# Optimization experiments

Hardware: AMD Instinct MI355X
Metric: run time of the kernel (lower is better)

Reference implementation:

```python
import jax, jax.numpy as jnp
import numpy as np

B, T_IN, T_OUT, N, FEAT = 32, 96, 96, 512, 8
HID = 512
GRID_SIZE, SPLINE_ORDER = 5, 3
GRID_RANGE = (-1.0, 1.0)


def _make_grid():
    # matches KANLinear.create_grid: identical row per in_feature, so keep 1-D
    h = (GRID_RANGE[1] - GRID_RANGE[0]) / GRID_SIZE
    return jnp.arange(-SPLINE_ORDER, GRID_SIZE + SPLINE_ORDER + 1, dtype=jnp.float32) * h + GRID_RANGE[0]


def _b_splines(x, grid):
    # x: [M, in_features]; de Boor-Cox recursion, order SPLINE_ORDER
    x = x[..., None]  # [M, in, 1]
    bases = ((x >= grid[:-1]) & (x < grid[1:])).astype(x.dtype)
    for k in range(1, SPLINE_ORDER + 1):
        left = (x - grid[:-(k + 1)]) / (grid[k:-1] - grid[:-(k + 1)])
        right = (grid[k + 1:] - x) / (grid[k + 1:] - grid[1:-k])
        bases = left * bases[..., :-1] + right * bases[..., 1:]
    return bases  # [M, in, grid_size + spline_order]


def setup_inputs() -> dict:
    key = jax.random.key(0)
    ks = jax.random.split(key, 12)
    s = 0.05
    return {
        "X": jax.random.normal(ks[0], (B, T_IN, N, FEAT), jnp.float32),
        "Y": jax.random.normal(ks[1], (B, T_OUT, N, FEAT), jnp.float32),
        "Wx": jax.random.normal(ks[2], (HID, T_IN * FEAT), jnp.float32) * s,
        "bx": jax.random.normal(ks[3], (HID,), jnp.float32) * s,
        "Wy": jax.random.normal(ks[4], (HID, T_OUT * FEAT), jnp.float32) * s,
        "by": jax.random.normal(ks[5], (HID,), jnp.float32) * s,
        "base_w": jax.random.normal(ks[6], (64, 2 * HID), jnp.float32) * s,
        "spline_w": jax.random.normal(ks[7], (64, 2 * HID, GRID_SIZE + SPLINE_ORDER), jnp.float32) * s,
        "spline_scaler": jax.random.normal(ks[8], (64, 2 * HID), jnp.float32) * s,
        "Wf": jax.random.normal(ks[9], (T_OUT * FEAT, 64), jnp.float32) * s,
        "bf": jax.random.normal(ks[10], (T_OUT * FEAT,), jnp.float32) * s,
    }


def reference(X, Y, Wx, bx, Wy, by, base_w, spline_w, spline_scaler, Wf, bf):
    # [B, T, N, F] -> [B, N, T*F]
    Xf = jnp.transpose(X, (0, 2, 1, 3)).reshape(B, N, T_IN * FEAT)
    Yf = jnp.transpose(Y, (0, 2, 1, 3)).reshape(B, N, T_OUT * FEAT)
    Hx = jnp.tanh(Xf @ Wx.T + bx)
    Hy = jnp.tanh(Yf @ Wy.T + by)
    h = jnp.concatenate([Hx, Hy], axis=-1).reshape(B * N, 2 * HID)

    grid = _make_grid()
    base_out = jax.nn.silu(h) @ base_w.T
    scaled_sw = spline_w * spline_scaler[..., None]  # [out, in, coeff]
    spline_out = jnp.einsum("mik,oik->mo", _b_splines(h, grid), scaled_sw)
    kan_out = (base_out + spline_out).reshape(B, N, 64)

    out = kan_out @ Wf.T + bf  # [B, N, T_OUT*FEAT]
    out = out.reshape(B, N, T_OUT, FEAT)
    return jnp.transpose(out, (0, 2, 1, 3))  # [B, T_OUT, N, FEAT]
```

## Files before the change

kernel.cpp:

```cpp
#include <hip/hip_runtime.h>
#include <cmath>

#define B_    32
#define T_    96
#define N_    512
#define F_    8
#define TF_   768
#define HID_  512
#define M_    16384
#define KIN_  1024
#define KS_   8

typedef short short8 __attribute__((ext_vector_type(8)));
typedef float f32x4  __attribute__((ext_vector_type(4)));
typedef unsigned int  uintx4 __attribute__((ext_vector_type(4)));
typedef unsigned long long ulongx2 __attribute__((ext_vector_type(2)));
typedef _Float16 halfx8 __attribute__((ext_vector_type(8)));
typedef unsigned short      ushort_t;
typedef unsigned int        uint_t;
typedef unsigned long long  ulong_t;

#define HT_B     0ull
#define WQ_B     33554432ull
#define WB_B     34734080ull
#define SH_B     36306944ull
#define KANR_B   61472768ull
#define WFQ_B    63569920ull

static __device__ inline uint_t  fbits(float f){ return __builtin_bit_cast(uint_t, f); }
static __device__ inline ushort_t f2b(float f){
    uint_t u = fbits(f);
    return (ushort_t)((u + 0x7fffu + ((u >> 16) & 1u)) >> 16);
}
static __device__ inline float b2f(ushort_t h){ return __builtin_bit_cast(float, (uint_t)h << 16); }
static __device__ inline ulong_t pack4(float4 v){
    return (ulong_t)f2b(v.x) | ((ulong_t)f2b(v.y) << 16) |
           ((ulong_t)f2b(v.z) << 32) | ((ulong_t)f2b(v.w) << 48);
}
static __device__ inline ulong_t pack4t(float4 v){
    uint_t d0 = (fbits(v.x) >> 16) | (fbits(v.y) & 0xffff0000u);
    uint_t d1 = (fbits(v.z) >> 16) | (fbits(v.w) & 0xffff0000u);
    return (ulong_t)d0 | ((ulong_t)d1 << 32);
}
static __device__ inline float fast_tanh(float x){
    const float e = __expf(2.0f * x);
    return 1.0f - 2.0f / (e + 1.0f);
}
static __device__ inline void gload_lds16(const void* g, void* l){
    __builtin_amdgcn_global_load_lds(
        (const __attribute__((address_space(1))) unsigned int*)g,
        (__attribute__((address_space(3))) unsigned int*)l, 16, 0, 0);
}

__global__ __launch_bounds__(256) void pack_wq(
    const float* __restrict__ base_w,
    const float* __restrict__ spline_w,
    const float* __restrict__ scaler,
    ushort_t* __restrict__ wq)
{
    const int e = blockIdx.x * 256 + threadIdx.x;
    const int j    = e & 7;
    const int ln   = (e >> 3) & 63;
    const int ct   = (e >> 9) & 3;
    const int t    = (e >> 11) & 3;
    const int rest = e >> 13;
    const int ss   = rest % 9;
    const int ks   = rest / 9;
    const int o = ct * 16 + (ln & 15);
    const int g = ln >> 4;
    float v;
    if (ss < 8) {
        const int i = ks * 128 + ss * 16 + t * 4 + g;
        v = spline_w[(o * KIN_ + i) * 8 + j] * scaler[o * KIN_ + i];
    } else {
        const int i = ks * 128 + t * 32 + g * 8 + j;
        v = base_w[o * KIN_ + i];
    }
    wq[e] = f2b(v);
}

__global__ __launch_bounds__(256) void pack_wb2(
    const float* __restrict__ Wx,
    const float* __restrict__ Wy,
    ushort_t* __restrict__ wb)
{
    const int e = blockIdx.x * 256 + threadIdx.x;
    const float v = (e < 512 * TF_) ? Wx[e] : Wy[e - 512 * TF_];
    wb[e] = f2b(v);
}

__global__ __launch_bounds__(256) void pack_wfq(
    const float* __restrict__ Wf, ushort_t* __restrict__ wfq)
{
    const int e = blockIdx.x * 256 + threadIdx.x;
    const int jj  = e & 7;
    const int ln  = (e >> 3) & 63;
    const int rt  = (e >> 9) & 3;
    const int s   = (e >> 11) & 1;
    const int wvt = (e >> 12) & 1;
    const int tb  = e >> 13;
    const int tf = tb * 128 + wvt * 64 + rt * 16 + (ln & 15);
    const int o  = s * 32 + (ln >> 4) * 8 + jj;
    wfq[e] = f2b(Wf[(size_t)tf * 64 + o]);
}

__global__ __launch_bounds__(256) void xcvt_kernel(
    const float* __restrict__ Xs, ushort_t* __restrict__ xbf)
{
    __shared__ __align__(16) char lds[32 * 1552];
    const int tid = threadIdx.x;
    const int n0  = blockIdx.x * 32;
    const int bb  = blockIdx.y;
    const int nl  = (tid & 63) >> 1;
    const int f4  = (tid & 1) * 4;
    const int tq  = tid >> 6;
    #pragma unroll 4
    for (int u = 0; u < 24; u++) {
        const int t = u * 4 + tq;
        const float4 v = *(const float4*)(Xs + (size_t)bb * (T_ * N_ * F_)
                                             + (size_t)t * (N_ * F_)
                                             + (size_t)(n0 + nl) * F_ + f4);
        *(ulong_t*)(lds + nl * 1552 + t * 16 + f4 * 2) = pack4t(v);
    }
    __syncthreads();
    #pragma unroll 4
    for (int u = 0; u < 12; u++) {
        const int c   = u * 256 + tid;
        const int row = c / 96;
        const int col = c - row * 96;
        const uintx4 val = *(const uintx4*)(lds + row * 1552 + col * 16);
        *(uintx4*)(xbf + (size_t)(bb * 512 + n0 + row) * TF_ + col * 8) = val;
    }
}

__global__ __launch_bounds__(512, 2) void gemm_tanh_v7(
    const ushort_t* __restrict__ xbf,
    const ushort_t* __restrict__ wb,
    const float* __restrict__ bias,
    ushort_t* __restrict__ ht, int z)
{
    __shared__ __align__(16) char smem[32768];

    const int tid = threadIdx.x;
    const int wv  = tid >> 6;
    const int ln  = tid & 63;
    const int lr  = ln & 15;
    const int hi  = ln >> 4;
    const int wm  = wv >> 2;
    const int wj  = wv & 3;

    const int m0  = blockIdx.x * 128;
    const int jl0 = blockIdx.y * 128;
    const int j0  = z * 512 + jl0;

    const int r_l = ln >> 3;
    const int ck  = ((ln & 7) ^ r_l) * 8;

    f32x4 acc[4][2] = {};

    for (int kt = 0; kt < 12; kt++) {
        __syncthreads();
        #pragma unroll
        for (int s = 0; s < 2; s++) {
            const int reg = s * 8 + wv;
            const int row = reg * 8 + r_l;
            gload_lds16(xbf + (size_t)(m0 + row) * TF_ + kt * 64 + ck,
                        smem + reg * 1024 + ln * 16);
            gload_lds16(wb + (size_t)(j0 + row) * TF_ + kt * 64 + ck,
                        smem + 16384 + reg * 1024 + ln * 16);
        }
        __syncthreads();

        #pragma unroll
        for (int h = 0; h < 2; h++) {
            const int g = h * 4 + hi;
            short8 a[4], b[2];
            #pragma unroll
            for (int rt = 0; rt < 4; rt++) {
                const int r = wm * 64 + rt * 16 + lr;
                a[rt] = *(short8*)(smem + r * 128 + ((g ^ (r & 7)) * 16));
            }
            #pragma unroll
            for (int ct = 0; ct < 2; ct++) {
                const int r = wj * 32 + ct * 16 + lr;
                b[ct] = *(short8*)(smem + 16384 + r * 128 + ((g ^ (r & 7)) * 16));
            }
            #pragma unroll
            for (int rt = 0; rt < 4; rt++)
                #pragma unroll
                for (int ct = 0; ct < 2; ct++)
                    acc[rt][ct] = __builtin_amdgcn_mfma_f32_16x16x32_bf16(
                        a[rt], b[ct], acc[rt][ct], 0, 0, 0);
        }
    }

    __syncthreads();
    #pragma unroll
    for (int ct = 0; ct < 2; ct++) {
        const int j = wj * 32 + ct * 16 + lr;
        const float bvv = bias[jl0 + j];
        #pragma unroll
        for (int rt = 0; rt < 4; rt++) {
            const f32x4 v = acc[rt][ct];
            float4 tv;
            tv.x = fast_tanh(v[0] + bvv);
            tv.y = fast_tanh(v[1] + bvv);
            tv.z = fast_tanh(v[2] + bvv);
            tv.w = fast_tanh(v[3] + bvv);
            const int slot = wm * 8 + rt * 2 + (hi >> 1);
            *(ulong_t*)(smem + j * 256 + ((slot ^ (j & 15)) * 16) + (hi & 1) * 8)
                = pack4(tv);
        }
    }
    __syncthreads();
    {
        const int j  = tid >> 2;
        const int q4 = tid & 3;
        ushort_t* dst = ht + (size_t)(j0 + j) * M_ + m0 + q4 * 32;
        #pragma unroll
        for (int w = 0; w < 4; w++) {
            const int slot = q4 * 4 + w;
            short8 val = *(short8*)(smem + j * 256 + ((slot ^ (j & 15)) * 16));
            *(short8*)(dst + w * 8) = val;
        }
    }
}

static __device__ inline short8 eval_bases(float x)
{
    const float v = fmaf(x, 2.5f, 2.5f);
    float sf = floorf(v);
    sf = fminf(fmaxf(sf, 0.0f), 4.0f);
    const float u = v - sf;
    const int si = (int)sf;
    const float u2 = u * u, u3 = u2 * u;
    const float omu = 1.0f - u;
    const float omu3 = omu * omu * omu;
    const float Bb0 = omu3 * (1.0f / 6.0f);
    const float Bb3 = u3 * (1.0f / 6.0f);
    const float Bb1 = fmaf(0.5f, u3, 2.0f / 3.0f) - u2;
    const float Bb2 = 1.0f - Bb0 - Bb1 - Bb3;
    const uint_t d0 = (fbits(Bb0) >> 16) | (fbits(Bb1) & 0xffff0000u);
    const uint_t d1 = (fbits(Bb2) >> 16) | (fbits(Bb3) & 0xffff0000u);
    const ulong_t P = (ulong_t)d0 | ((ulong_t)d1 << 32);
    const int sh = si << 4;
    const ulong_t Plo = P << (sh & 63);
    const ulong_t Phi = P >> ((64 - sh) & 63);
    ulongx2 pr;
    pr.x = (si == 4) ? 0ull : Plo;
    pr.y = (si == 0) ? 0ull : ((si == 4) ? P : Phi);
    return __builtin_bit_cast(short8, pr);
}

__global__ __launch_bounds__(256) void kan_v5(
    const ushort_t* __restrict__ ht,
    const ushort_t* __restrict__ wq,
    _Float16* __restrict__ kanp)
{
    const int tid = threadIdx.x;
    const int wv  = tid >> 6;
    const int ln  = tid & 63;
    const int g   = ln >> 4;
    const int lr  = ln & 15;
    const int m0  = blockIdx.x * 64;
    const int ks  = blockIdx.y;
    const int iB  = ks * 128;
    const size_t r0 = (size_t)(m0 + wv * 16 + lr);

    const short8* wqf = (const short8*)wq + (size_t)ks * 9216 + ln;
    const ushort_t* htg  = ht + (size_t)(iB + g) * M_ + r0;
    const ushort_t* htg8 = ht + (size_t)(iB + g * 8) * M_ + r0;

    f32x4 acc[4] = {};

    for (int ss = 0; ss < 8; ss++) {
        #pragma unroll
        for (int t = 0; t < 4; t++) {
            const short8* bp = wqf + (size_t)(ss * 4 + t) * 256;
            const short8 b0 = bp[0], b1 = bp[64], b2 = bp[128], b3 = bp[192];
            const short8 a0 = eval_bases(b2f(htg[(size_t)(ss * 16 + t * 4) * M_]));
            acc[0] = __builtin_amdgcn_mfma_f32_16x16x32_bf16(a0, b0, acc[0], 0, 0, 0);
            acc[1] = __builtin_amdgcn_mfma_f32_16x16x32_bf16(a0, b1, acc[1], 0, 0, 0);
            acc[2] = __builtin_amdgcn_mfma_f32_16x16x32_bf16(a0, b2, acc[2], 0, 0, 0);
            acc[3] = __builtin_amdgcn_mfma_f32_16x16x32_bf16(a0, b3, acc[3], 0, 0, 0);
        }
    }
    #pragma unroll
    for (int t = 0; t < 4; t++) {
        const short8* bp = wqf + (size_t)(32 + t) * 256;
        const short8 b0 = bp[0], b1 = bp[64], b2 = bp[128], b3 = bp[192];
        uintx4 d;
        #pragma unroll
        for (int jj = 0; jj < 4; jj++) {
            const float x0 = b2f(htg8[(size_t)(t * 32 + 2 * jj)     * M_]);
            const float x1 = b2f(htg8[(size_t)(t * 32 + 2 * jj + 1) * M_]);
            const float s0 = x0 / (1.0f + __expf(-x0));
            const float s1 = x1 / (1.0f + __expf(-x1));
            d[jj] = (fbits(s0) >> 16) | (fbits(s1) & 0xffff0000u);
        }
        const short8 a0 = __builtin_bit_cast(short8, d);
        acc[0] = __builtin_amdgcn_mfma_f32_16x16x32_bf16(a0, b0, acc[0], 0, 0, 0);
        acc[1] = __builtin_amdgcn_mfma_f32_16x16x32_bf16(a0, b1, acc[1], 0, 0, 0);
        acc[2] = __builtin_amdgcn_mfma_f32_16x16x32_bf16(a0, b2, acc[2], 0, 0, 0);
        acc[3] = __builtin_amdgcn_mfma_f32_16x16x32_bf16(a0, b3, acc[3], 0, 0, 0);
    }

    #pragma unroll
    for (int ct = 0; ct < 4; ct++) {
        const int o = ct * 16 + lr;
        #pragma unroll
        for (int q = 0; q < 4; q++) {
            const size_t row = (size_t)(m0 + wv * 16 + g * 4 + q);
            kanp[(size_t)ks * (M_ * 64) + row * 64 + o] = (_Float16)acc[ct][q];
        }
    }
}

__global__ __launch_bounds__(256) void reduce_kan(
    const _Float16* __restrict__ kanp, ushort_t* __restrict__ kanr)
{
    const int e8 = blockIdx.x * 256 + threadIdx.x;
    const size_t base = (size_t)e8 * 8;
    float s[8] = {};
    #pragma unroll
    for (int p = 0; p < KS_; p++) {
        const halfx8 v = *(const halfx8*)(kanp + (size_t)p * (M_ * 64) + base);
        #pragma unroll
        for (int j = 0; j < 8; j++) s[j] += (float)v[j];
    }
    float4 s0 = make_float4(s[0], s[1], s[2], s[3]);
    float4 s1 = make_float4(s[4], s[5], s[6], s[7]);
    ulongx2 outv;
    outv.x = pack4(s0);
    outv.y = pack4(s1);
    *(ulongx2*)(kanr + base) = outv;
}

__global__ __launch_bounds__(256) void final_v2(
    const ushort_t* __restrict__ kanr,
    const ushort_t* __restrict__ wfq,
    const float* __restrict__ bf,
    float* __restrict__ out)
{
    const int tid = threadIdx.x;
    const int wv  = tid >> 6;
    const int ln  = tid & 63;
    const int lr  = ln & 15;
    const int hi  = ln >> 4;
    const int wvm = wv >> 1;
    const int wvt = wv & 1;
    const int mb  = blockIdx.x;
    const int tb  = blockIdx.y;

    f32x4 acc[4][4] = {};

    #pragma unroll
    for (int s = 0; s < 2; s++) {
        short8 afr[4], bfr[4];
        #pragma unroll
        for (int rt = 0; rt < 4; rt++) {
            const size_t idx = ((size_t)(((tb * 2 + wvt) * 2 + s) * 4 + rt)) * 64 + ln;
            afr[rt] = ((const short8*)wfq)[idx];
        }
        #pragma unroll
        for (int ct = 0; ct < 4; ct++) {
            const int m = mb * 128 + wvm * 64 + ct * 16 + lr;
            bfr[ct] = *(const short8*)(kanr + (size_t)m * 64 + s * 32 + hi * 8);
        }
        #pragma unroll
        for (int rt = 0; rt < 4; rt++)
            #pragma unroll
            for (int ct = 0; ct < 4; ct++)
                acc[rt][ct] = __builtin_amdgcn_mfma_f32_16x16x32_bf16(
                    afr[rt], bfr[ct], acc[rt][ct], 0, 0, 0);
    }

    #pragma unroll
    for (int rt = 0; rt < 4; rt++) {
        const int tf0 = tb * 128 + wvt * 64 + rt * 16 + hi * 4;
        const float4 b4 = *(const float4*)&bf[tf0];
        const int t  = tf0 >> 3;
        const int f0 = tf0 & 7;
        #pragma unroll
        for (int ct = 0; ct < 4; ct++) {
            const int m = mb * 128 + wvm * 64 + ct * 16 + lr;
            const int bb = m >> 9;
            const int n  = m & 511;
            const f32x4 v = acc[rt][ct];
            float4 o4 = make_float4(v[0] + b4.x, v[1] + b4.y, v[2] + b4.z, v[3] + b4.w);
            *(float4*)&out[(size_t)bb * (T_ * N_ * F_)
                           + (size_t)t * (N_ * F_)
                           + (size_t)n * F_ + f0] = o4;
        }
    }
}

extern "C" void kernel_launch(void* const* d_in, const int* in_sizes, int n_in,
                              void* d_out, int out_size, void* d_ws, size_t ws_size,
                              hipStream_t stream)
{
    const float* X      = (const float*)d_in[0];
    const float* Y      = (const float*)d_in[1];
    const float* Wx     = (const float*)d_in[2];
    const float* bx     = (const float*)d_in[3];
    const float* Wy     = (const float*)d_in[4];
    const float* by     = (const float*)d_in[5];
    const float* base_w = (const float*)d_in[6];
    const float* spline_w = (const float*)d_in[7];
    const float* spline_scaler = (const float*)d_in[8];
    const float* Wf     = (const float*)d_in[9];
    const float* bf     = (const float*)d_in[10];

    float* out = (float*)d_out;
    ushort_t* ht   = (ushort_t*)((char*)d_ws + HT_B);
    ushort_t* wq   = (ushort_t*)((char*)d_ws + WQ_B);
    ushort_t* wb   = (ushort_t*)((char*)d_ws + WB_B);
    ushort_t* xbf  = (ushort_t*)((char*)d_ws + SH_B);
    _Float16* kanp = (_Float16*)((char*)d_ws + SH_B);
    ushort_t* kanr = (ushort_t*)((char*)d_ws + KANR_B);
    ushort_t* wfq  = (ushort_t*)((char*)d_ws + WFQ_B);

    pack_wq<<<2304, 256, 0, stream>>>(base_w, spline_w, spline_scaler, wq);
    pack_wb2<<<3072, 256, 0, stream>>>(Wx, Wy, wb);
    pack_wfq<<<192, 256, 0, stream>>>(Wf, wfq);

    xcvt_kernel<<<dim3(16, 32), 256, 0, stream>>>(X, xbf);
    gemm_tanh_v7<<<dim3(128, 4), 512, 0, stream>>>(xbf, wb, bx, ht, 0);
    xcvt_kernel<<<dim3(16, 32), 256, 0, stream>>>(Y, xbf);
    gemm_tanh_v7<<<dim3(128, 4), 512, 0, stream>>>(xbf, wb, by, ht, 1);

    kan_v5<<<dim3(M_ / 64, KS_), 256, 0, stream>>>(ht, wq, kanp);
    reduce_kan<<<512, 256, 0, stream>>>(kanp, kanr);
    final_v2<<<dim3(128, 6), 256, 0, stream>>>(kanr, wfq, bf, out);
}
```

Before: 144.6 us.

## Stage KAN weights in LDS, double row tile, fold split-K reduction into final GEMM

Result: slower. 151.9 us (+5.0%).

```diff
diff --git a/kernel.cpp b/kernel.cpp
--- a/kernel.cpp
+++ b/kernel.cpp
@@ -12,10 +12,10 @@
 #define KS_   8
 
 typedef short short8 __attribute__((ext_vector_type(8)));
+typedef _Float16 half8 __attribute__((ext_vector_type(8)));
 typedef float f32x4  __attribute__((ext_vector_type(4)));
 typedef unsigned int  uintx4 __attribute__((ext_vector_type(4)));
 typedef unsigned long long ulongx2 __attribute__((ext_vector_type(2)));
-typedef _Float16 halfx8 __attribute__((ext_vector_type(8)));
 typedef unsigned short      ushort_t;
 typedef unsigned int        uint_t;
 typedef unsigned long long  ulong_t;
@@ -24,7 +24,6 @@
 #define WQ_B     33554432ull
 #define WB_B     34734080ull
 #define SH_B     36306944ull
-#define KANR_B   61472768ull
 #define WFQ_B    63569920ull
 
 static __device__ inline uint_t  fbits(float f){ return __builtin_bit_cast(uint_t, f); }
@@ -89,8 +88,8 @@
     wb[e] = f2b(v);
 }
 
-__global__ __launch_bounds__(256) void pack_wfq(
-    const float* __restrict__ Wf, ushort_t* __restrict__ wfq)
+__global__ __launch_bounds__(256) void pack_wfq16(
+    const float* __restrict__ Wf, _Float16* __restrict__ wfq)
 {
     const int e = blockIdx.x * 256 + threadIdx.x;
     const int jj  = e & 7;
@@ -101,7 +100,7 @@
     const int tb  = e >> 13;
     const int tf = tb * 128 + wvt * 64 + rt * 16 + (ln & 15);
     const int o  = s * 32 + (ln >> 4) * 8 + jj;
-    wfq[e] = f2b(Wf[(size_t)tf * 64 + o]);
+    wfq[e] = (_Float16)Wf[(size_t)tf * 64 + o];
 }
 
 __global__ __launch_bounds__(256) void xcvt_kernel(
@@ -230,7 +229,7 @@
 {
     const float v = fmaf(x, 2.5f, 2.5f);
     float sf = floorf(v);
-    sf = fminf(fmaxf(sf, 0.0f), 4.0f);
+    sf = fminf(sf, 4.0f);
     const float u = v - sf;
     const int si = (int)sf;
     const float u2 = u * u, u3 = u2 * u;
@@ -252,93 +251,96 @@
     return __builtin_bit_cast(short8, pr);
 }
 
-__global__ __launch_bounds__(256) void kan_v5(
+__global__ __launch_bounds__(256) void kan_v7(
     const ushort_t* __restrict__ ht,
     const ushort_t* __restrict__ wq,
     _Float16* __restrict__ kanp)
 {
+    __shared__ __align__(16) char sb[4096];
+
     const int tid = threadIdx.x;
     const int wv  = tid >> 6;
     const int ln  = tid & 63;
     const int g   = ln >> 4;
     const int lr  = ln & 15;
-    const int m0  = blockIdx.x * 64;
+    const int m0  = blockIdx.x * 128;
     const int ks  = blockIdx.y;
     const int iB  = ks * 128;
-    const size_t r0 = (size_t)(m0 + wv * 16 + lr);
-
-    const short8* wqf = (const short8*)wq + (size_t)ks * 9216 + ln;
-    const ushort_t* htg  = ht + (size_t)(iB + g) * M_ + r0;
-    const ushort_t* htg8 = ht + (size_t)(iB + g * 8) * M_ + r0;
-
-    f32x4 acc[4] = {};
-
-    for (int ss = 0; ss < 8; ss++) {
-        #pragma unroll
-        for (int t = 0; t < 4; t++) {
-            const short8* bp = wqf + (size_t)(ss * 4 + t) * 256;
-            const short8 b0 = bp[0], b1 = bp[64], b2 = bp[128], b3 = bp[192];
-            const short8 a0 = eval_bases(b2f(htg[(size_t)(ss * 16 + t * 4) * M_]));
-            acc[0] = __builtin_amdgcn_mfma_f32_16x16x32_bf16(a0, b0, acc[0], 0, 0, 0);
-            acc[1] = __builtin_amdgcn_mfma_f32_16x16x32_bf16(a0, b1, acc[1], 0, 0, 0);
-            acc[2] = __builtin_amdgcn_mfma_f32_16x16x32_bf16(a0, b2, acc[2], 0, 0, 0);
-            acc[3] = __builtin_amdgcn_mfma_f32_16x16x32_bf16(a0, b3, acc[3], 0, 0, 0);
-        }
-    }
+    const size_t r0 = (size_t)(m0 + wv * 32 + lr);
+
+    const ushort_t* wqk = wq + (size_t)ks * 73728;
+    const ushort_t* hpA = ht + (size_t)(iB + g) * M_ + r0;
+    const ushort_t* hpS = ht + (size_t)(iB + g * 8) * M_ + r0;
+
+    f32x4 acc[2][4] = {};
+
+    gload_lds16(wqk + (size_t)wv * 512 + ln * 8, sb + wv * 1024 + ln * 16);
+    __syncthreads();
+
     #pragma unroll
-    for (int t = 0; t < 4; t++) {
-        const short8* bp = wqf + (size_t)(32 + t) * 256;
-        const short8 b0 = bp[0], b1 = bp[64], b2 = bp[128], b3 = bp[192];
-        uintx4 d;
-        #pragma unroll
-        for (int jj = 0; jj < 4; jj++) {
-            const float x0 = b2f(htg8[(size_t)(t * 32 + 2 * jj)     * M_]);
-            const float x1 = b2f(htg8[(size_t)(t * 32 + 2 * jj + 1) * M_]);
-            const float s0 = x0 / (1.0f + __expf(-x0));
-            const float s1 = x1 / (1.0f + __expf(-x1));
-            d[jj] = (fbits(s0) >> 16) | (fbits(s1) & 0xffff0000u);
-        }
-        const short8 a0 = __builtin_bit_cast(short8, d);
-        acc[0] = __builtin_amdgcn_mfma_f32_16x16x32_bf16(a0, b0, acc[0], 0, 0, 0);
-        acc[1] = __builtin_amdgcn_mfma_f32_16x16x32_bf16(a0, b1, acc[1], 0, 0, 0);
-        acc[2] = __builtin_amdgcn_mfma_f32_16x16x32_bf16(a0, b2, acc[2], 0, 0, 0);
-        acc[3] = __builtin_amdgcn_mfma_f32_16x16x32_bf16(a0, b3, acc[3], 0, 0, 0);
+    for (int it = 0; it < 36; ++it) {
+        const short8 b0 = *(short8*)(sb + 0 * 1024 + ln * 16);
+        const short8 b1 = *(short8*)(sb + 1 * 1024 + ln * 16);
+        const short8 b2 = *(short8*)(sb + 2 * 1024 + ln * 16);
+        const short8 b3 = *(short8*)(sb + 3 * 1024 + ln * 16);
+        __syncthreads();
+        if (it < 35)
+            gload_lds16(wqk + (size_t)((it + 1) * 4 + wv) * 512 + ln * 8,
+                        sb + wv * 1024 + ln * 16);
+
+        short8 a0, a1;
+        if (it < 32) {
+            const size_t off = (size_t)(4 * it) * M_;
+            a0 = eval_bases(b2f(hpA[off]));
+            a1 = eval_bases(b2f(hpA[off + 16]));
+        } else {
+            const int t = it - 32;
+            uintx4 d0v, d1v;
+            #pragma unroll
+            for (int jj = 0; jj < 4; jj++) {
+                const size_t o0 = (size_t)(t * 32 + 2 * jj) * M_;
+                const size_t o1 = (size_t)(t * 32 + 2 * jj + 1) * M_;
+                const float x0 = b2f(hpS[o0]),      x1 = b2f(hpS[o1]);
+                const float y0 = b2f(hpS[o0 + 16]), y1 = b2f(hpS[o1 + 16]);
+                const float s0 = x0 / (1.0f + __expf(-x0));
+                const float s1 = x1 / (1.0f + __expf(-x1));
+                const float u0 = y0 / (1.0f + __expf(-y0));
+                const float u1 = y1 / (1.0f + __expf(-y1));
+                d0v[jj] = (fbits(s0) >> 16) | (fbits(s1) & 0xffff0000u);
+                d1v[jj] = (fbits(u0) >> 16) | (fbits(u1) & 0xffff0000u);
+            }
+            a0 = __builtin_bit_cast(short8, d0v);
+            a1 = __builtin_bit_cast(short8, d1v);
+        }
+
+        acc[0][0] = __builtin_amdgcn_mfma_f32_16x16x32_bf16(a0, b0, acc[0][0], 0, 0, 0);
+        acc[0][1] = __builtin_amdgcn_mfma_f32_16x16x32_bf16(a0, b1, acc[0][1], 0, 0, 0);
+        acc[0][2] = __builtin_amdgcn_mfma_f32_16x16x32_bf16(a0, b2, acc[0][2], 0, 0, 0);
+        acc[0][3] = __builtin_amdgcn_mfma_f32_16x16x32_bf16(a0, b3, acc[0][3], 0, 0, 0);
+        acc[1][0] = __builtin_amdgcn_mfma_f32_16x16x32_bf16(a1, b0, acc[1][0], 0, 0, 0);
+        acc[1][1] = __builtin_amdgcn_mfma_f32_16x16x32_bf16(a1, b1, acc[1][1], 0, 0, 0);
+        acc[1][2] = __builtin_amdgcn_mfma_f32_16x16x32_bf16(a1, b2, acc[1][2], 0, 0, 0);
+        acc[1][3] = __builtin_amdgcn_mfma_f32_16x16x32_bf16(a1, b3, acc[1][3], 0, 0, 0);
+        __syncthreads();
     }
 
     #pragma unroll
-    for (int ct = 0; ct < 4; ct++) {
-        const int o = ct * 16 + lr;
-        #pragma unroll
-        for (int q = 0; q < 4; q++) {
-            const size_t row = (size_t)(m0 + wv * 16 + g * 4 + q);
-            kanp[(size_t)ks * (M_ * 64) + row * 64 + o] = (_Float16)acc[ct][q];
-        }
-    }
-}
-
-__global__ __launch_bounds__(256) void reduce_kan(
-    const _Float16* __restrict__ kanp, ushort_t* __restrict__ kanr)
-{
-    const int e8 = blockIdx.x * 256 + threadIdx.x;
-    const size_t base = (size_t)e8 * 8;
-    float s[8] = {};
-    #pragma unroll
-    for (int p = 0; p < KS_; p++) {
-        const halfx8 v = *(const halfx8*)(kanp + (size_t)p * (M_ * 64) + base);
-        #pragma unroll
-        for (int j = 0; j < 8; j++) s[j] += (float)v[j];
-    }
-    float4 s0 = make_float4(s[0], s[1], s[2], s[3]);
-    float4 s1 = make_float4(s[4], s[5], s[6], s[7]);
-    ulongx2 outv;
-    outv.x = pack4(s0);
-    outv.y = pack4(s1);
-    *(ulongx2*)(kanr + base) = outv;
-}
-
-__global__ __launch_bounds__(256) void final_v2(
-    const ushort_t* __restrict__ kanr,
-    const ushort_t* __restrict__ wfq,
+    for (int rt = 0; rt < 2; rt++) {
+        #pragma unroll
+        for (int ct = 0; ct < 4; ct++) {
+            const int o = ct * 16 + lr;
+            #pragma unroll
+            for (int q = 0; q < 4; q++) {
+                const size_t row = (size_t)(m0 + wv * 32 + rt * 16 + g * 4 + q);
+                kanp[(size_t)ks * (M_ * 64) + row * 64 + o] = (_Float16)acc[rt][ct][q];
+            }
+        }
+    }
+}
+
+__global__ __launch_bounds__(256) void final_v3(
+    const _Float16* __restrict__ kanp,
+    const _Float16* __restrict__ wfq,
     const float* __restrict__ bf,
     float* __restrict__ out)
 {
@@ -356,22 +358,27 @@
 
     #pragma unroll
     for (int s = 0; s < 2; s++) {
-        short8 afr[4], bfr[4];
+        half8 afr[4], bfr[4];
         #pragma unroll
         for (int rt = 0; rt < 4; rt++) {
             const size_t idx = ((size_t)(((tb * 2 + wvt) * 2 + s) * 4 + rt)) * 64 + ln;
-            afr[rt] = ((const short8*)wfq)[idx];
+            afr[rt] = ((const half8*)wfq)[idx];
         }
         #pragma unroll
         for (int ct = 0; ct < 4; ct++) {
             const int m = mb * 128 + wvm * 64 + ct * 16 + lr;
-            bfr[ct] = *(const short8*)(kanr + (size_t)m * 64 + s * 32 + hi * 8);
+            const _Float16* bp = kanp + (size_t)m * 64 + s * 32 + hi * 8;
+            half8 sum = *(const half8*)bp;
+            #pragma unroll
+            for (int p = 1; p < KS_; p++)
+                sum += *(const half8*)(bp + (size_t)p * (M_ * 64));
+            bfr[ct] = sum;
         }
         #pragma unroll
         for (int rt = 0; rt < 4; rt++)
             #pragma unroll
             for (int ct = 0; ct < 4; ct++)
-                acc[rt][ct] = __builtin_amdgcn_mfma_f32_16x16x32_bf16(
+                acc[rt][ct] = __builtin_amdgcn_mfma_f32_16x16x32_f16(
                     afr[rt], bfr[ct], acc[rt][ct], 0, 0, 0);
     }
 
@@ -417,19 +424,17 @@
     ushort_t* wb   = (ushort_t*)((char*)d_ws + WB_B);
     ushort_t* xbf  = (ushort_t*)((char*)d_ws + SH_B);
     _Float16* kanp = (_Float16*)((char*)d_ws + SH_B);
-    ushort_t* kanr = (ushort_t*)((char*)d_ws + KANR_B);
-    ushort_t* wfq  = (ushort_t*)((char*)d_ws + WFQ_B);
+    _Float16* wfq  = (_Float16*)((char*)d_ws + WFQ_B);
 
     pack_wq<<<2304, 256, 0, stream>>>(base_w, spline_w, spline_scaler, wq);
     pack_wb2<<<3072, 256, 0, stream>>>(Wx, Wy, wb);
-    pack_wfq<<<192, 256, 0, stream>>>(Wf, wfq);
+    pack_wfq16<<<192, 256, 0, stream>>>(Wf, wfq);
 
     xcvt_kernel<<<dim3(16, 32), 256, 0, stream>>>(X, xbf);
     gemm_tanh_v7<<<dim3(128, 4), 512, 0, stream>>>(xbf, wb, bx, ht, 0);
     xcvt_kernel<<<dim3(16, 32), 256, 0, stream>>>(Y, xbf);
     gemm_tanh_v7<<<dim3(128, 4), 512, 0, stream>>>(xbf, wb, by, ht, 1);
 
-    kan_v5<<<dim3(M_ / 64, KS_), 256, 0, stream>>>(ht, wq, kanp);
-    reduce_kan<<<512, 256, 0, stream>>>(kanp, kanr);
-    final_v2<<<dim3(128, 6), 256, 0, stream>>>(kanr, wfq, bf, out);
-}
+    kan_v7<<<dim3(M_ / 128, KS_), 256, 0, stream>>>(ht, wq, kanp);
+    final_v3<<<dim3(128, 6), 256, 0, stream>>>(kanp, wfq, bf, out);
+}
```

## Stage KAN activations and weights in LDS, double the row tile per block

Applied to the files above, without the earlier changes.

After: 138.7 us. 4.1% less time.

```diff
diff --git a/kernel.cpp b/kernel.cpp
--- a/kernel.cpp
+++ b/kernel.cpp
@@ -12,10 +12,10 @@
 #define KS_   8
 
 typedef short short8 __attribute__((ext_vector_type(8)));
+typedef _Float16 halfx8 __attribute__((ext_vector_type(8)));
 typedef float f32x4  __attribute__((ext_vector_type(4)));
 typedef unsigned int  uintx4 __attribute__((ext_vector_type(4)));
 typedef unsigned long long ulongx2 __attribute__((ext_vector_type(2)));
-typedef _Float16 halfx8 __attribute__((ext_vector_type(8)));
 typedef unsigned short      ushort_t;
 typedef unsigned int        uint_t;
 typedef unsigned long long  ulong_t;
@@ -230,7 +230,7 @@
 {
     const float v = fmaf(x, 2.5f, 2.5f);
     float sf = floorf(v);
-    sf = fminf(fmaxf(sf, 0.0f), 4.0f);
+    sf = fminf(sf, 4.0f);
     const float u = v - sf;
     const int si = (int)sf;
     const float u2 = u * u, u3 = u2 * u;
@@ -252,66 +252,103 @@
     return __builtin_bit_cast(short8, pr);
 }
 
-__global__ __launch_bounds__(256) void kan_v5(
+__global__ __launch_bounds__(256) void kan_v8(
     const ushort_t* __restrict__ ht,
     const ushort_t* __restrict__ wq,
     _Float16* __restrict__ kanp)
 {
+    __shared__ __align__(16) char lds[40960];
+
     const int tid = threadIdx.x;
     const int wv  = tid >> 6;
     const int ln  = tid & 63;
     const int g   = ln >> 4;
     const int lr  = ln & 15;
-    const int m0  = blockIdx.x * 64;
+    const int m0  = blockIdx.x * 128;
     const int ks  = blockIdx.y;
     const int iB  = ks * 128;
-    const size_t r0 = (size_t)(m0 + wv * 16 + lr);
-
-    const short8* wqf = (const short8*)wq + (size_t)ks * 9216 + ln;
-    const ushort_t* htg  = ht + (size_t)(iB + g) * M_ + r0;
-    const ushort_t* htg8 = ht + (size_t)(iB + g * 8) * M_ + r0;
-
-    f32x4 acc[4] = {};
-
-    for (int ss = 0; ss < 8; ss++) {
-        #pragma unroll
-        for (int t = 0; t < 4; t++) {
-            const short8* bp = wqf + (size_t)(ss * 4 + t) * 256;
-            const short8 b0 = bp[0], b1 = bp[64], b2 = bp[128], b3 = bp[192];
-            const short8 a0 = eval_bases(b2f(htg[(size_t)(ss * 16 + t * 4) * M_]));
-            acc[0] = __builtin_amdgcn_mfma_f32_16x16x32_bf16(a0, b0, acc[0], 0, 0, 0);
-            acc[1] = __builtin_amdgcn_mfma_f32_16x16x32_bf16(a0, b1, acc[1], 0, 0, 0);
-            acc[2] = __builtin_amdgcn_mfma_f32_16x16x32_bf16(a0, b2, acc[2], 0, 0, 0);
-            acc[3] = __builtin_amdgcn_mfma_f32_16x16x32_bf16(a0, b3, acc[3], 0, 0, 0);
-        }
-    }
-    #pragma unroll
-    for (int t = 0; t < 4; t++) {
-        const short8* bp = wqf + (size_t)(32 + t) * 256;
-        const short8 b0 = bp[0], b1 = bp[64], b2 = bp[128], b3 = bp[192];
-        uintx4 d;
-        #pragma unroll
-        for (int jj = 0; jj < 4; jj++) {
-            const float x0 = b2f(htg8[(size_t)(t * 32 + 2 * jj)     * M_]);
-            const float x1 = b2f(htg8[(size_t)(t * 32 + 2 * jj + 1) * M_]);
-            const float s0 = x0 / (1.0f + __expf(-x0));
-            const float s1 = x1 / (1.0f + __expf(-x1));
-            d[jj] = (fbits(s0) >> 16) | (fbits(s1) & 0xffff0000u);
-        }
-        const short8 a0 = __builtin_bit_cast(short8, d);
-        acc[0] = __builtin_amdgcn_mfma_f32_16x16x32_bf16(a0, b0, acc[0], 0, 0, 0);
-        acc[1] = __builtin_amdgcn_mfma_f32_16x16x32_bf16(a0, b1, acc[1], 0, 0, 0);
-        acc[2] = __builtin_amdgcn_mfma_f32_16x16x32_bf16(a0, b2, acc[2], 0, 0, 0);
-        acc[3] = __builtin_amdgcn_mfma_f32_16x16x32_bf16(a0, b3, acc[3], 0, 0, 0);
-    }
-
-    #pragma unroll
-    for (int ct = 0; ct < 4; ct++) {
-        const int o = ct * 16 + lr;
-        #pragma unroll
-        for (int q = 0; q < 4; q++) {
-            const size_t row = (size_t)(m0 + wv * 16 + g * 4 + q);
-            kanp[(size_t)ks * (M_ * 64) + row * 64 + o] = (_Float16)acc[ct][q];
+
+    const ushort_t* wqk = wq + (size_t)ks * 73728;
+
+    #pragma unroll
+    for (int c = 0; c < 8; c++) {
+        const int ll = wv * 8 + c;
+        const int il = ll * 4 + (ln >> 4);
+        const int r8 = (ln & 15) * 8;
+        gload_lds16(ht + (size_t)(iB + il) * M_ + m0 + r8,
+                    lds + ll * 1024 + ln * 16);
+    }
+    gload_lds16(wqk + (size_t)wv * 512 + ln * 8,
+                lds + 32768 + wv * 1024 + ln * 16);
+    __syncthreads();
+
+    const int hbA = g * 256  + wv * 64 + lr * 2;
+    const int hbS = g * 2048 + wv * 64 + lr * 2;
+
+    f32x4 acc[2][4] = {};
+
+    #pragma unroll
+    for (int it = 0; it < 36; ++it) {
+        const int p = it & 1;
+        char* sb = lds + 32768 + p * 4096;
+        const short8 b0 = *(short8*)(sb + 0 * 1024 + ln * 16);
+        const short8 b1 = *(short8*)(sb + 1 * 1024 + ln * 16);
+        const short8 b2 = *(short8*)(sb + 2 * 1024 + ln * 16);
+        const short8 b3 = *(short8*)(sb + 3 * 1024 + ln * 16);
+
+        if (it < 35)
+            gload_lds16(wqk + (size_t)((it + 1) * 4 + wv) * 512 + ln * 8,
+                        lds + 32768 + (p ^ 1) * 4096 + wv * 1024 + ln * 16);
+
+        short8 a0, a1;
+        if (it < 32) {
+            const int off = hbA + ((it >> 2) * 16 + (it & 3) * 4) * 256;
+            a0 = eval_bases(b2f(*(const ushort_t*)(lds + off)));
+            a1 = eval_bases(b2f(*(const ushort_t*)(lds + off + 32)));
+        } else {
+            const int t = it - 32;
+            uintx4 d0v, d1v;
+            #pragma unroll
+            for (int jj = 0; jj < 4; jj++) {
+                const int o0 = hbS + (t * 32 + 2 * jj) * 256;
+                const int o1 = o0 + 256;
+                const float x0 = b2f(*(const ushort_t*)(lds + o0));
+                const float x1 = b2f(*(const ushort_t*)(lds + o1));
+                const float y0 = b2f(*(const ushort_t*)(lds + o0 + 32));
+                const float y1 = b2f(*(const ushort_t*)(lds + o1 + 32));
+                const float s0 = x0 / (1.0f + __expf(-x0));
+                const float s1 = x1 / (1.0f + __expf(-x1));
+                const float u0 = y0 / (1.0f + __expf(-y0));
+                const float u1 = y1 / (1.0f + __expf(-y1));
+                d0v[jj] = (fbits(s0) >> 16) | (fbits(s1) & 0xffff0000u);
+                d1v[jj] = (fbits(u0) >> 16) | (fbits(u1) & 0xffff0000u);
+            }
+            a0 = __builtin_bit_cast(short8, d0v);
+            a1 = __builtin_bit_cast(short8, d1v);
+        }
+
+        acc[0][0] = __builtin_amdgcn_mfma_f32_16x16x32_bf16(a0, b0, acc[0][0], 0, 0, 0);
+        acc[0][1] = __builtin_amdgcn_mfma_f32_16x16x32_bf16(a0, b1, acc[0][1], 0, 0, 0);
+        acc[0][2] = __builtin_amdgcn_mfma_f32_16x16x32_bf16(a0, b2, acc[0][2], 0, 0, 0);
+        acc[0][3] = __builtin_amdgcn_mfma_f32_16x16x32_bf16(a0, b3, acc[0][3], 0, 0, 0);
+        acc[1][0] = __builtin_amdgcn_mfma_f32_16x16x32_bf16(a1, b0, acc[1][0], 0, 0, 0);
+        acc[1][1] = __builtin_amdgcn_mfma_f32_16x16x32_bf16(a1, b1, acc[1][1], 0, 0, 0);
+        acc[1][2] = __builtin_amdgcn_mfma_f32_16x16x32_bf16(a1, b2, acc[1][2], 0, 0, 0);
+        acc[1][3] = __builtin_amdgcn_mfma_f32_16x16x32_bf16(a1, b3, acc[1][3], 0, 0, 0);
+
+        __syncthreads();
+    }
+
+    #pragma unroll
+    for (int rt = 0; rt < 2; rt++) {
+        #pragma unroll
+        for (int ct = 0; ct < 4; ct++) {
+            const int o = ct * 16 + lr;
+            #pragma unroll
+            for (int q = 0; q < 4; q++) {
+                const size_t row = (size_t)(m0 + wv * 32 + rt * 16 + g * 4 + q);
+                kanp[(size_t)ks * (M_ * 64) + row * 64 + o] = (_Float16)acc[rt][ct][q];
+            }
         }
     }
 }
@@ -429,7 +466,7 @@
     xcvt_kernel<<<dim3(16, 32), 256, 0, stream>>>(Y, xbf);
     gemm_tanh_v7<<<dim3(128, 4), 512, 0, stream>>>(xbf, wb, by, ht, 1);
 
-    kan_v5<<<dim3(M_ / 64, KS_), 256, 0, stream>>>(ht, wq, kanp);
+    kan_v8<<<dim3(M_ / 128, KS_), 256, 0, stream>>>(ht, wq, kanp);
     reduce_kan<<<512, 256, 0, stream>>>(kanp, kanr);
     final_v2<<<dim3(128, 6), 256, 0, stream>>>(kanr, wfq, bf, out);
 }
```
